# Kernel optimization log

Hardware: AMD Instinct MI355X
Metric: run time of the kernel (lower is better)

The kernel has to match this reference:

```python
import jax, jax.numpy as jnp
import numpy as np

N = 50000       # number of nodes in the batch
K = 32          # max neighbors (padded)
D = 64          # embed_dim
V = 100000      # number of users (u2e vocab)


def setup_inputs() -> dict:
    key = jax.random.key(0)
    ks = jax.random.split(key, 10)
    nodes = jax.random.randint(ks[0], (N,), 0, V)
    neigh_idx = jax.random.randint(ks[1], (N, K), 0, V)
    counts = jax.random.randint(ks[2], (N,), 1, K + 1)          # ragged lengths, >=1
    neigh_mask = jnp.arange(K)[None, :] < counts[:, None]        # [N,K] bool
    u2e = jax.random.normal(ks[3], (V, D), dtype=jnp.float32) * 0.02
    s1 = 1.0 / np.sqrt(2 * D)
    s2 = 1.0 / np.sqrt(D)
    W1 = jax.random.normal(ks[4], (2 * D, D), dtype=jnp.float32) * s1
    b1 = jnp.zeros((D,), dtype=jnp.float32)
    W2 = jax.random.normal(ks[5], (D, D), dtype=jnp.float32) * s2
    b2 = jnp.zeros((D,), dtype=jnp.float32)
    W3 = jax.random.normal(ks[6], (D, 1), dtype=jnp.float32) * s2
    b3 = jnp.zeros((1,), dtype=jnp.float32)
    return {"u2e": u2e, "W1": W1, "b1": b1, "W2": W2, "b2": b2,
            "W3": W3, "b3": b3, "nodes": nodes, "neigh_idx": neigh_idx,
            "neigh_mask": neigh_mask}


def reference(u2e, W1, b1, W2, b2, W3, b3, nodes, neigh_idx, neigh_mask):
    # Gather neighbor and center-node embeddings (the per-node loop, vectorized)
    e_u = u2e[neigh_idx]                                   # [N,K,D]
    u_rep = u2e[nodes]                                     # [N,D]
    # GraphRec attention MLP on concat([neighbor, center]) -> scalar score
    x = jnp.concatenate(
        [e_u, jnp.broadcast_to(u_rep[:, None, :], e_u.shape)], axis=-1)  # [N,K,2D]
    h = jax.nn.relu(x @ W1 + b1)                           # [N,K,D]
    h = jax.nn.relu(h @ W2 + b2)                           # [N,K,D]
    scores = (h @ W3 + b3)[..., 0]                         # [N,K]
    neg = jnp.asarray(-1e9, dtype=scores.dtype)
    att = jax.nn.softmax(jnp.where(neigh_mask, scores, neg), axis=-1)  # [N,K]
    att = att * neigh_mask.astype(att.dtype)
    # att_history = (e_u^T @ att)^T, per node: weighted neighbor sum
    out = jnp.einsum('nk,nkd->nd', att, e_u)               # [N,D]
    return out
```

## Files before the change

kernel.cpp:

```cpp
#include <hip/hip_runtime.h>
#include <hip/hip_bf16.h>

typedef __bf16 bf16x8 __attribute__((ext_vector_type(8)));
typedef __bf16 bf16x4 __attribute__((ext_vector_type(4)));
typedef float  f32x4  __attribute__((ext_vector_type(4)));

__global__ void init_flag_kernel(int* flag) { *flag = 0; }

__global__ void detect_mask_kernel(const unsigned* __restrict__ mw, int nwords,
                                   int* __restrict__ flag) {
    int any = 0;
    for (int i = blockIdx.x * blockDim.x + threadIdx.x; i < nwords;
         i += gridDim.x * blockDim.x)
        if (mw[i] > 1u) any = 1;
    if (__any(any)) {
        if ((threadIdx.x & 63) == 0) atomicOr(flag, 1);
    }
}

__global__ __launch_bounds__(256) void graphrec_agg_kernel(
    const float* __restrict__ u2e,
    const float* __restrict__ W1, const float* __restrict__ b1,
    const float* __restrict__ W2, const float* __restrict__ b2,
    const float* __restrict__ W3, const float* __restrict__ b3,
    const int* __restrict__ nodes, const int* __restrict__ neigh_idx,
    const void* __restrict__ mask, const int* __restrict__ flag,
    float* __restrict__ out, int N)
{
    __shared__ __align__(16) __bf16 w1f[16][64][8];
    __shared__ __align__(16) __bf16 w2f[8][64][8];
    __shared__ __align__(16) float  eu[4][32][64];
    __shared__ __align__(16) __bf16 afrag[4][2][2][64][8];
    __shared__ __align__(16) __bf16 urep[4][64];
    __shared__ float att_s[4][32];

    const int tid = threadIdx.x;
    const int w = tid >> 6;
    const int l = tid & 63;
    const int g = l >> 4;
    const int c = l & 15;

    for (int f = w; f < 16; f += 4) {
        int kt = f >> 2, nt = f & 3;
        int r0 = kt * 32 + g * 8, col = nt * 16 + c;
        bf16x8 t;
        #pragma unroll
        for (int i = 0; i < 8; ++i) t[i] = (__bf16)W1[(r0 + i) * 64 + col];
        *(bf16x8*)&w1f[f][l][0] = t;
    }
    for (int f = w; f < 8; f += 4) {
        int kt = f >> 2, nt = f & 3;
        int r0 = kt * 32 + g * 8, col = nt * 16 + c;
        bf16x8 t;
        #pragma unroll
        for (int i = 0; i < 8; ++i) t[i] = (__bf16)W2[(r0 + i) * 64 + col];
        *(bf16x8*)&w2f[f][l][0] = t;
    }
    __syncthreads();

    float b1v[4], b2v[4], w3v[4];
    #pragma unroll
    for (int nt = 0; nt < 4; ++nt) {
        b1v[nt] = b1[nt * 16 + c];
        b2v[nt] = b2[nt * 16 + c];
        w3v[nt] = W3[nt * 16 + c];
    }
    const float b3s = b3[0];
    const int layout8 = *flag;
    const unsigned char* m8p  = (const unsigned char*)mask;
    const int*           m32p = (const int*)mask;

    for (int n = blockIdx.x * 4 + w; n < N; n += gridDim.x * 4) {
        int vidx = 0;
        if (l < 32) vidx = neigh_idx[n * 32 + l];
        bool mv = false;
        if (l < 32) mv = layout8 ? (m8p[n * 32 + l] != 0)
                                 : (m32p[n * 32 + l] != 0);
        unsigned long long bal = __ballot(mv);

        int un = nodes[n];
        float ur = u2e[(size_t)un * 64 + l];
        urep[w][l] = (__bf16)ur;

        #pragma unroll
        for (int kb = 0; kb < 8; ++kb) {
            int k = kb * 4 + g;
            int idx = __shfl(vidx, k);
            f32x4 v = *(const f32x4*)(u2e + (size_t)idx * 64 + c * 4);
            *(f32x4*)&eu[w][k][c * 4] = v;
            int d0 = c * 4;
            bf16x4 bv;
            bv[0] = (__bf16)v[0]; bv[1] = (__bf16)v[1];
            bv[2] = (__bf16)v[2]; bv[3] = (__bf16)v[3];
            int lanep = (k & 15) + (((d0 & 31) >> 3) << 4);
            *(bf16x4*)&afrag[w][k >> 4][d0 >> 5][lanep][d0 & 7] = bv;
        }

        #pragma unroll
        for (int mt = 0; mt < 2; ++mt) {
            bf16x8 a0 = *(const bf16x8*)&afrag[w][mt][0][l][0];
            bf16x8 a1 = *(const bf16x8*)&afrag[w][mt][1][l][0];
            bf16x8 a2 = *(const bf16x8*)&urep[w][g * 8];
            bf16x8 a3 = *(const bf16x8*)&urep[w][32 + g * 8];
            #pragma unroll
            for (int nt = 0; nt < 4; ++nt) {
                f32x4 cc = {0.f, 0.f, 0.f, 0.f};
                cc = __builtin_amdgcn_mfma_f32_16x16x32_bf16(a0, *(const bf16x8*)&w1f[0 + nt][l][0], cc, 0, 0, 0);
                cc = __builtin_amdgcn_mfma_f32_16x16x32_bf16(a1, *(const bf16x8*)&w1f[4 + nt][l][0], cc, 0, 0, 0);
                cc = __builtin_amdgcn_mfma_f32_16x16x32_bf16(a2, *(const bf16x8*)&w1f[8 + nt][l][0], cc, 0, 0, 0);
                cc = __builtin_amdgcn_mfma_f32_16x16x32_bf16(a3, *(const bf16x8*)&w1f[12 + nt][l][0], cc, 0, 0, 0);
                #pragma unroll
                for (int r = 0; r < 4; ++r) {
                    float hv = fmaxf(cc[r] + b1v[nt], 0.f);
                    int lanep = g * 4 + r + ((((nt & 1) << 1) + (c >> 3)) << 4);
                    afrag[w][mt][nt >> 1][lanep][c & 7] = (__bf16)hv;
                }
            }
        }

        float p[2][4];
        #pragma unroll
        for (int mt = 0; mt < 2; ++mt) {
            bf16x8 a0 = *(const bf16x8*)&afrag[w][mt][0][l][0];
            bf16x8 a1 = *(const bf16x8*)&afrag[w][mt][1][l][0];
            float pr0 = 0.f, pr1 = 0.f, pr2 = 0.f, pr3 = 0.f;
            #pragma unroll
            for (int nt = 0; nt < 4; ++nt) {
                f32x4 cc = {0.f, 0.f, 0.f, 0.f};
                cc = __builtin_amdgcn_mfma_f32_16x16x32_bf16(a0, *(const bf16x8*)&w2f[0 + nt][l][0], cc, 0, 0, 0);
                cc = __builtin_amdgcn_mfma_f32_16x16x32_bf16(a1, *(const bf16x8*)&w2f[4 + nt][l][0], cc, 0, 0, 0);
                pr0 += fmaxf(cc[0] + b2v[nt], 0.f) * w3v[nt];
                pr1 += fmaxf(cc[1] + b2v[nt], 0.f) * w3v[nt];
                pr2 += fmaxf(cc[2] + b2v[nt], 0.f) * w3v[nt];
                pr3 += fmaxf(cc[3] + b2v[nt], 0.f) * w3v[nt];
            }
            p[mt][0] = pr0; p[mt][1] = pr1; p[mt][2] = pr2; p[mt][3] = pr3;
        }

        float s[8];
        #pragma unroll
        for (int m = 0; m < 8; ++m) {
            float v = p[m >> 2][m & 3];
            v += __shfl_xor(v, 1);
            v += __shfl_xor(v, 2);
            v += __shfl_xor(v, 4);
            v += __shfl_xor(v, 8);
            s[m] = v + b3s;
        }

        bool vald[8];
        float m8 = -1e30f;
        #pragma unroll
        for (int m = 0; m < 8; ++m) {
            int k = (m >> 2) * 16 + g * 4 + (m & 3);
            vald[m] = ((bal >> k) & 1ull) != 0;
            if (vald[m]) m8 = fmaxf(m8, s[m]);
        }
        m8 = fmaxf(m8, __shfl_xor(m8, 16));
        m8 = fmaxf(m8, __shfl_xor(m8, 32));
        float es[8], ls = 0.f;
        #pragma unroll
        for (int m = 0; m < 8; ++m) {
            es[m] = vald[m] ? __expf(s[m] - m8) : 0.f;
            ls += es[m];
        }
        ls += __shfl_xor(ls, 16);
        ls += __shfl_xor(ls, 32);
        float inv = (ls > 0.f) ? 1.f / ls : 0.f;
        if (c == 0) {
            #pragma unroll
            for (int m = 0; m < 8; ++m) {
                int k = (m >> 2) * 16 + g * 4 + (m & 3);
                att_s[w][k] = es[m] * inv;
            }
        }

        float acc = 0.f;
        #pragma unroll
        for (int k = 0; k < 32; ++k)
            acc += att_s[w][k] * eu[w][k][l];
        out[(size_t)n * 64 + l] = acc;
    }
}

extern "C" void kernel_launch(void* const* d_in, const int* in_sizes, int n_in,
                              void* d_out, int out_size, void* d_ws, size_t ws_size,
                              hipStream_t stream) {
    const float* u2e = (const float*)d_in[0];
    const float* W1  = (const float*)d_in[1];
    const float* b1  = (const float*)d_in[2];
    const float* W2  = (const float*)d_in[3];
    const float* b2  = (const float*)d_in[4];
    const float* W3  = (const float*)d_in[5];
    const float* b3  = (const float*)d_in[6];
    const int* nodes     = (const int*)d_in[7];
    const int* neigh_idx = (const int*)d_in[8];
    const void* mask     = d_in[9];

    const int N = in_sizes[7];
    int* flag = (int*)d_ws;

    init_flag_kernel<<<1, 1, 0, stream>>>(flag);
    int nwords = in_sizes[9] / 4;
    if (nwords > 100000) nwords = 100000;
    detect_mask_kernel<<<128, 256, 0, stream>>>((const unsigned*)mask, nwords, flag);

    graphrec_agg_kernel<<<1024, 256, 0, stream>>>(
        u2e, W1, b1, W2, b2, W3, b3, nodes, neigh_idx, mask, flag,
        (float*)d_out, N);
}
```

Measured before the change: 217.7 us.

## Gather neighbors from a bf16 copy of the embedding table with prefetched indices

Adds a pre-pass converting u2e to bf16 in workspace, so neighbor gathers read half the bytes. Shared memory is reorganized into padded row-major bf16 tiles, and W2 fragments move into registers. The next node's indices and mask are prefetched one iteration ahead. Grid and launch bounds change, and the flag reset becomes a memset. The final weighted sum now uses bf16 neighbor values, which lowers output precision.

```diff
diff --git a/kernel.cpp b/kernel.cpp
--- a/kernel.cpp
+++ b/kernel.cpp
@@ -4,8 +4,6 @@
 typedef __bf16 bf16x8 __attribute__((ext_vector_type(8)));
 typedef __bf16 bf16x4 __attribute__((ext_vector_type(4)));
 typedef float  f32x4  __attribute__((ext_vector_type(4)));
-
-__global__ void init_flag_kernel(int* flag) { *flag = 0; }
 
 __global__ void detect_mask_kernel(const unsigned* __restrict__ mw, int nwords,
                                    int* __restrict__ flag) {
@@ -18,8 +16,24 @@
     }
 }
 
-__global__ __launch_bounds__(256) void graphrec_agg_kernel(
-    const float* __restrict__ u2e,
+__global__ void cvt_bf16_kernel(const float* __restrict__ src,
+                                __bf16* __restrict__ dst, int n) {
+    for (int i = (blockIdx.x * blockDim.x + threadIdx.x) * 8; i < n;
+         i += gridDim.x * blockDim.x * 8) {
+        f32x4 a = *(const f32x4*)(src + i);
+        f32x4 b = *(const f32x4*)(src + i + 4);
+        bf16x8 o;
+        o[0] = (__bf16)a[0]; o[1] = (__bf16)a[1];
+        o[2] = (__bf16)a[2]; o[3] = (__bf16)a[3];
+        o[4] = (__bf16)b[0]; o[5] = (__bf16)b[1];
+        o[6] = (__bf16)b[2]; o[7] = (__bf16)b[3];
+        *(bf16x8*)(dst + i) = o;
+    }
+}
+
+template <int BF16SRC>
+__global__ __launch_bounds__(256, 3) void graphrec_agg_kernel(
+    const float* __restrict__ u2e, const __bf16* __restrict__ tbl,
     const float* __restrict__ W1, const float* __restrict__ b1,
     const float* __restrict__ W2, const float* __restrict__ b2,
     const float* __restrict__ W3, const float* __restrict__ b3,
@@ -28,9 +42,8 @@
     float* __restrict__ out, int N)
 {
     __shared__ __align__(16) __bf16 w1f[16][64][8];
-    __shared__ __align__(16) __bf16 w2f[8][64][8];
-    __shared__ __align__(16) float  eu[4][32][64];
-    __shared__ __align__(16) __bf16 afrag[4][2][2][64][8];
+    __shared__ __align__(16) __bf16 eu16[4][32][72];
+    __shared__ __align__(16) __bf16 h1s[4][32][72];
     __shared__ __align__(16) __bf16 urep[4][64];
     __shared__ float att_s[4][32];
 
@@ -48,15 +61,16 @@
         for (int i = 0; i < 8; ++i) t[i] = (__bf16)W1[(r0 + i) * 64 + col];
         *(bf16x8*)&w1f[f][l][0] = t;
     }
-    for (int f = w; f < 8; f += 4) {
+    __syncthreads();
+
+    bf16x8 w2r[8];
+    #pragma unroll
+    for (int f = 0; f < 8; ++f) {
         int kt = f >> 2, nt = f & 3;
         int r0 = kt * 32 + g * 8, col = nt * 16 + c;
-        bf16x8 t;
-        #pragma unroll
-        for (int i = 0; i < 8; ++i) t[i] = (__bf16)W2[(r0 + i) * 64 + col];
-        *(bf16x8*)&w2f[f][l][0] = t;
-    }
-    __syncthreads();
+        #pragma unroll
+        for (int i = 0; i < 8; ++i) w2r[f][i] = (__bf16)W2[(r0 + i) * 64 + col];
+    }
 
     float b1v[4], b2v[4], w3v[4];
     #pragma unroll
@@ -70,38 +84,67 @@
     const unsigned char* m8p  = (const unsigned char*)mask;
     const int*           m32p = (const int*)mask;
 
-    for (int n = blockIdx.x * 4 + w; n < N; n += gridDim.x * 4) {
-        int vidx = 0;
-        if (l < 32) vidx = neigh_idx[n * 32 + l];
-        bool mv = false;
-        if (l < 32) mv = layout8 ? (m8p[n * 32 + l] != 0)
-                                 : (m32p[n * 32 + l] != 0);
+    const int stride = gridDim.x * 4;
+    int n = blockIdx.x * 4 + w;
+
+    int vidx = 0, un = 0;
+    bool mv = false;
+    if (n < N) {
+        if (l < 32) {
+            vidx = neigh_idx[n * 32 + l];
+            mv = layout8 ? (m8p[n * 32 + l] != 0) : (m32p[n * 32 + l] != 0);
+        }
+        un = nodes[n];
+    }
+
+    for (; n < N; n += stride) {
+        int n2 = n + stride;
+        int vidx2 = 0, un2 = 0;
+        bool mv2 = false;
+        if (n2 < N) {
+            if (l < 32) {
+                vidx2 = neigh_idx[n2 * 32 + l];
+                mv2 = layout8 ? (m8p[n2 * 32 + l] != 0) : (m32p[n2 * 32 + l] != 0);
+            }
+            un2 = nodes[n2];
+        }
+
         unsigned long long bal = __ballot(mv);
 
-        int un = nodes[n];
-        float ur = u2e[(size_t)un * 64 + l];
-        urep[w][l] = (__bf16)ur;
-
-        #pragma unroll
-        for (int kb = 0; kb < 8; ++kb) {
-            int k = kb * 4 + g;
-            int idx = __shfl(vidx, k);
-            f32x4 v = *(const f32x4*)(u2e + (size_t)idx * 64 + c * 4);
-            *(f32x4*)&eu[w][k][c * 4] = v;
-            int d0 = c * 4;
-            bf16x4 bv;
-            bv[0] = (__bf16)v[0]; bv[1] = (__bf16)v[1];
-            bv[2] = (__bf16)v[2]; bv[3] = (__bf16)v[3];
-            int lanep = (k & 15) + (((d0 & 31) >> 3) << 4);
-            *(bf16x4*)&afrag[w][k >> 4][d0 >> 5][lanep][d0 & 7] = bv;
-        }
-
+        if (BF16SRC) {
+            urep[w][l] = tbl[(size_t)un * 64 + l];
+        } else {
+            urep[w][l] = (__bf16)u2e[(size_t)un * 64 + l];
+        }
+
+        if (BF16SRC) {
+            #pragma unroll
+            for (int it = 0; it < 4; ++it) {
+                int k = it * 8 + (l >> 3);
+                int idx = __shfl(vidx, k);
+                bf16x8 v = *(const bf16x8*)(tbl + (size_t)idx * 64 + (l & 7) * 8);
+                *(bf16x8*)&eu16[w][k][(l & 7) * 8] = v;
+            }
+        } else {
+            #pragma unroll
+            for (int it = 0; it < 8; ++it) {
+                int k = it * 4 + g;
+                int idx = __shfl(vidx, k);
+                f32x4 v = *(const f32x4*)(u2e + (size_t)idx * 64 + c * 4);
+                bf16x4 bv;
+                bv[0] = (__bf16)v[0]; bv[1] = (__bf16)v[1];
+                bv[2] = (__bf16)v[2]; bv[3] = (__bf16)v[3];
+                *(bf16x4*)&eu16[w][k][c * 4] = bv;
+            }
+        }
+
+        bf16x8 a2 = *(const bf16x8*)&urep[w][g * 8];
+        bf16x8 a3 = *(const bf16x8*)&urep[w][32 + g * 8];
         #pragma unroll
         for (int mt = 0; mt < 2; ++mt) {
-            bf16x8 a0 = *(const bf16x8*)&afrag[w][mt][0][l][0];
-            bf16x8 a1 = *(const bf16x8*)&afrag[w][mt][1][l][0];
-            bf16x8 a2 = *(const bf16x8*)&urep[w][g * 8];
-            bf16x8 a3 = *(const bf16x8*)&urep[w][32 + g * 8];
+            const __bf16* arow = &eu16[w][mt * 16 + c][0];
+            bf16x8 a0 = *(const bf16x8*)(arow + g * 8);
+            bf16x8 a1 = *(const bf16x8*)(arow + 32 + g * 8);
             #pragma unroll
             for (int nt = 0; nt < 4; ++nt) {
                 f32x4 cc = {0.f, 0.f, 0.f, 0.f};
@@ -112,8 +155,7 @@
                 #pragma unroll
                 for (int r = 0; r < 4; ++r) {
                     float hv = fmaxf(cc[r] + b1v[nt], 0.f);
-                    int lanep = g * 4 + r + ((((nt & 1) << 1) + (c >> 3)) << 4);
-                    afrag[w][mt][nt >> 1][lanep][c & 7] = (__bf16)hv;
+                    h1s[w][mt * 16 + g * 4 + r][nt * 16 + c] = (__bf16)hv;
                 }
             }
         }
@@ -121,14 +163,15 @@
         float p[2][4];
         #pragma unroll
         for (int mt = 0; mt < 2; ++mt) {
-            bf16x8 a0 = *(const bf16x8*)&afrag[w][mt][0][l][0];
-            bf16x8 a1 = *(const bf16x8*)&afrag[w][mt][1][l][0];
+            const __bf16* arow = &h1s[w][mt * 16 + c][0];
+            bf16x8 a0 = *(const bf16x8*)(arow + g * 8);
+            bf16x8 a1 = *(const bf16x8*)(arow + 32 + g * 8);
             float pr0 = 0.f, pr1 = 0.f, pr2 = 0.f, pr3 = 0.f;
             #pragma unroll
             for (int nt = 0; nt < 4; ++nt) {
                 f32x4 cc = {0.f, 0.f, 0.f, 0.f};
-                cc = __builtin_amdgcn_mfma_f32_16x16x32_bf16(a0, *(const bf16x8*)&w2f[0 + nt][l][0], cc, 0, 0, 0);
-                cc = __builtin_amdgcn_mfma_f32_16x16x32_bf16(a1, *(const bf16x8*)&w2f[4 + nt][l][0], cc, 0, 0, 0);
+                cc = __builtin_amdgcn_mfma_f32_16x16x32_bf16(a0, w2r[0 + nt], cc, 0, 0, 0);
+                cc = __builtin_amdgcn_mfma_f32_16x16x32_bf16(a1, w2r[4 + nt], cc, 0, 0, 0);
                 pr0 += fmaxf(cc[0] + b2v[nt], 0.f) * w3v[nt];
                 pr1 += fmaxf(cc[1] + b2v[nt], 0.f) * w3v[nt];
                 pr2 += fmaxf(cc[2] + b2v[nt], 0.f) * w3v[nt];
@@ -178,8 +221,10 @@
         float acc = 0.f;
         #pragma unroll
         for (int k = 0; k < 32; ++k)
-            acc += att_s[w][k] * eu[w][k][l];
+            acc += att_s[w][k] * (float)eu16[w][k][l];
         out[(size_t)n * 64 + l] = acc;
+
+        vidx = vidx2; mv = mv2; un = un2;
     }
 }
 
@@ -197,15 +242,26 @@
     const int* neigh_idx = (const int*)d_in[8];
     const void* mask     = d_in[9];
 
-    const int N = in_sizes[7];
+    const int N  = in_sizes[7];
+    const int VD = in_sizes[0];
+
     int* flag = (int*)d_ws;
-
-    init_flag_kernel<<<1, 1, 0, stream>>>(flag);
+    __bf16* tbl = (__bf16*)((char*)d_ws + 256);
+    const size_t needed = 256 + (size_t)VD * sizeof(__bf16);
+    const bool use16 = (ws_size >= needed);
+
+    hipMemsetAsync(flag, 0, sizeof(int), stream);
     int nwords = in_sizes[9] / 4;
-    if (nwords > 100000) nwords = 100000;
     detect_mask_kernel<<<128, 256, 0, stream>>>((const unsigned*)mask, nwords, flag);
 
-    graphrec_agg_kernel<<<1024, 256, 0, stream>>>(
-        u2e, W1, b1, W2, b2, W3, b3, nodes, neigh_idx, mask, flag,
-        (float*)d_out, N);
-}
+    if (use16) {
+        cvt_bf16_kernel<<<2048, 256, 0, stream>>>(u2e, tbl, VD);
+        graphrec_agg_kernel<1><<<768, 256, 0, stream>>>(
+            u2e, tbl, W1, b1, W2, b2, W3, b3, nodes, neigh_idx, mask, flag,
+            (float*)d_out, N);
+    } else {
+        graphrec_agg_kernel<0><<<768, 256, 0, stream>>>(
+            u2e, (const __bf16*)u2e, W1, b1, W2, b2, W3, b3, nodes, neigh_idx,
+            mask, flag, (float*)d_out, N);
+    }
+}
```

Result: slower. 319.9 us (+47.0%).

## Software-pipeline neighbor gathers and keep W2 and embeddings in registers

Applied to the files above, without the earlier changes.

Restructures the per-node loop into a software pipeline. The next node's neighbor embeddings and center embedding are loaded into registers while the current node's MLP runs, and index and mask loads are prefetched two nodes ahead. W2 fragments and the fp32 neighbor rows move from shared memory into registers, and the bf16 shared tile becomes a single padded row-major buffer, which shrinks LDS use. The final weighted sum is computed from registers with cross-lane shuffles. Launch bounds, grid size and the flag init (now a memset) also change, and the mask-detect scan loses its cap. The trade-offs are higher register pressure, which could limit occupancy, and a full scan of the mask.

```diff
diff --git a/kernel.cpp b/kernel.cpp
--- a/kernel.cpp
+++ b/kernel.cpp
@@ -4,8 +4,6 @@
 typedef __bf16 bf16x8 __attribute__((ext_vector_type(8)));
 typedef __bf16 bf16x4 __attribute__((ext_vector_type(4)));
 typedef float  f32x4  __attribute__((ext_vector_type(4)));
-
-__global__ void init_flag_kernel(int* flag) { *flag = 0; }
 
 __global__ void detect_mask_kernel(const unsigned* __restrict__ mw, int nwords,
                                    int* __restrict__ flag) {
@@ -18,7 +16,7 @@
     }
 }
 
-__global__ __launch_bounds__(256) void graphrec_agg_kernel(
+__global__ __launch_bounds__(256, 3) void graphrec_agg_kernel(
     const float* __restrict__ u2e,
     const float* __restrict__ W1, const float* __restrict__ b1,
     const float* __restrict__ W2, const float* __restrict__ b2,
@@ -28,9 +26,7 @@
     float* __restrict__ out, int N)
 {
     __shared__ __align__(16) __bf16 w1f[16][64][8];
-    __shared__ __align__(16) __bf16 w2f[8][64][8];
-    __shared__ __align__(16) float  eu[4][32][64];
-    __shared__ __align__(16) __bf16 afrag[4][2][2][64][8];
+    __shared__ __align__(16) __bf16 tile[4][32][72];
     __shared__ __align__(16) __bf16 urep[4][64];
     __shared__ float att_s[4][32];
 
@@ -48,15 +44,16 @@
         for (int i = 0; i < 8; ++i) t[i] = (__bf16)W1[(r0 + i) * 64 + col];
         *(bf16x8*)&w1f[f][l][0] = t;
     }
-    for (int f = w; f < 8; f += 4) {
+    __syncthreads();
+
+    bf16x8 w2r[8];
+    #pragma unroll
+    for (int f = 0; f < 8; ++f) {
         int kt = f >> 2, nt = f & 3;
         int r0 = kt * 32 + g * 8, col = nt * 16 + c;
-        bf16x8 t;
-        #pragma unroll
-        for (int i = 0; i < 8; ++i) t[i] = (__bf16)W2[(r0 + i) * 64 + col];
-        *(bf16x8*)&w2f[f][l][0] = t;
-    }
-    __syncthreads();
+        #pragma unroll
+        for (int i = 0; i < 8; ++i) w2r[f][i] = (__bf16)W2[(r0 + i) * 64 + col];
+    }
 
     float b1v[4], b2v[4], w3v[4];
     #pragma unroll
@@ -70,38 +67,77 @@
     const unsigned char* m8p  = (const unsigned char*)mask;
     const int*           m32p = (const int*)mask;
 
-    for (int n = blockIdx.x * 4 + w; n < N; n += gridDim.x * 4) {
-        int vidx = 0;
-        if (l < 32) vidx = neigh_idx[n * 32 + l];
-        bool mv = false;
-        if (l < 32) mv = layout8 ? (m8p[n * 32 + l] != 0)
-                                 : (m32p[n * 32 + l] != 0);
-        unsigned long long bal = __ballot(mv);
-
-        int un = nodes[n];
-        float ur = u2e[(size_t)un * 64 + l];
-        urep[w][l] = (__bf16)ur;
-
+    const int stride = gridDim.x * 4;
+    int nA = blockIdx.x * 4 + w;
+    int nB = nA + stride;
+
+    int vidxA = 0, unA = 0; bool mvA = false;
+    if (nA < N) {
+        if (l < 32) {
+            int o = nA * 32 + l;
+            vidxA = neigh_idx[o];
+            mvA = layout8 ? (m8p[o] != 0) : (m32p[o] != 0);
+        }
+        unA = nodes[nA];
+    }
+    int vidxB = 0, unB = 0; bool mvB = false;
+    if (nB < N) {
+        if (l < 32) {
+            int o = nB * 32 + l;
+            vidxB = neigh_idx[o];
+            mvB = layout8 ? (m8p[o] != 0) : (m32p[o] != 0);
+        }
+        unB = nodes[nB];
+    }
+
+    f32x4 rr[8]; float urv = 0.f;
+    if (nA < N) {
+        #pragma unroll
+        for (int kb = 0; kb < 8; ++kb) {
+            int idx = __shfl(vidxA, kb * 4 + g);
+            rr[kb] = *(const f32x4*)(u2e + (size_t)idx * 64 + c * 4);
+        }
+        urv = u2e[(size_t)unA * 64 + l];
+    }
+
+    for (; nA < N; nA += stride, nB += stride) {
+        int nC = nB + stride;
+        int vidxC = 0, unC = 0; bool mvC = false;
+        if (nC < N) {
+            if (l < 32) {
+                int o = nC * 32 + l;
+                vidxC = neigh_idx[o];
+                mvC = layout8 ? (m8p[o] != 0) : (m32p[o] != 0);
+            }
+            unC = nodes[nC];
+        }
+
+        unsigned long long bal = __ballot(mvA);
+        urep[w][l] = (__bf16)urv;
         #pragma unroll
         for (int kb = 0; kb < 8; ++kb) {
             int k = kb * 4 + g;
-            int idx = __shfl(vidx, k);
-            f32x4 v = *(const f32x4*)(u2e + (size_t)idx * 64 + c * 4);
-            *(f32x4*)&eu[w][k][c * 4] = v;
-            int d0 = c * 4;
             bf16x4 bv;
-            bv[0] = (__bf16)v[0]; bv[1] = (__bf16)v[1];
-            bv[2] = (__bf16)v[2]; bv[3] = (__bf16)v[3];
-            int lanep = (k & 15) + (((d0 & 31) >> 3) << 4);
-            *(bf16x4*)&afrag[w][k >> 4][d0 >> 5][lanep][d0 & 7] = bv;
-        }
-
+            bv[0] = (__bf16)rr[kb][0]; bv[1] = (__bf16)rr[kb][1];
+            bv[2] = (__bf16)rr[kb][2]; bv[3] = (__bf16)rr[kb][3];
+            *(bf16x4*)&tile[w][k][c * 4] = bv;
+        }
+
+        f32x4 rn[8]; float urvn;
+        #pragma unroll
+        for (int kb = 0; kb < 8; ++kb) {
+            int idx = __shfl(vidxB, kb * 4 + g);
+            rn[kb] = *(const f32x4*)(u2e + (size_t)idx * 64 + c * 4);
+        }
+        urvn = u2e[(size_t)unB * 64 + l];
+
+        bf16x8 a2 = *(const bf16x8*)&urep[w][g * 8];
+        bf16x8 a3 = *(const bf16x8*)&urep[w][32 + g * 8];
         #pragma unroll
         for (int mt = 0; mt < 2; ++mt) {
-            bf16x8 a0 = *(const bf16x8*)&afrag[w][mt][0][l][0];
-            bf16x8 a1 = *(const bf16x8*)&afrag[w][mt][1][l][0];
-            bf16x8 a2 = *(const bf16x8*)&urep[w][g * 8];
-            bf16x8 a3 = *(const bf16x8*)&urep[w][32 + g * 8];
+            const __bf16* arow = &tile[w][mt * 16 + c][0];
+            bf16x8 a0 = *(const bf16x8*)(arow + g * 8);
+            bf16x8 a1 = *(const bf16x8*)(arow + 32 + g * 8);
             #pragma unroll
             for (int nt = 0; nt < 4; ++nt) {
                 f32x4 cc = {0.f, 0.f, 0.f, 0.f};
@@ -112,8 +148,7 @@
                 #pragma unroll
                 for (int r = 0; r < 4; ++r) {
                     float hv = fmaxf(cc[r] + b1v[nt], 0.f);
-                    int lanep = g * 4 + r + ((((nt & 1) << 1) + (c >> 3)) << 4);
-                    afrag[w][mt][nt >> 1][lanep][c & 7] = (__bf16)hv;
+                    tile[w][mt * 16 + g * 4 + r][nt * 16 + c] = (__bf16)hv;
                 }
             }
         }
@@ -121,14 +156,15 @@
         float p[2][4];
         #pragma unroll
         for (int mt = 0; mt < 2; ++mt) {
-            bf16x8 a0 = *(const bf16x8*)&afrag[w][mt][0][l][0];
-            bf16x8 a1 = *(const bf16x8*)&afrag[w][mt][1][l][0];
+            const __bf16* arow = &tile[w][mt * 16 + c][0];
+            bf16x8 a0 = *(const bf16x8*)(arow + g * 8);
+            bf16x8 a1 = *(const bf16x8*)(arow + 32 + g * 8);
             float pr0 = 0.f, pr1 = 0.f, pr2 = 0.f, pr3 = 0.f;
             #pragma unroll
             for (int nt = 0; nt < 4; ++nt) {
                 f32x4 cc = {0.f, 0.f, 0.f, 0.f};
-                cc = __builtin_amdgcn_mfma_f32_16x16x32_bf16(a0, *(const bf16x8*)&w2f[0 + nt][l][0], cc, 0, 0, 0);
-                cc = __builtin_amdgcn_mfma_f32_16x16x32_bf16(a1, *(const bf16x8*)&w2f[4 + nt][l][0], cc, 0, 0, 0);
+                cc = __builtin_amdgcn_mfma_f32_16x16x32_bf16(a0, w2r[0 + nt], cc, 0, 0, 0);
+                cc = __builtin_amdgcn_mfma_f32_16x16x32_bf16(a1, w2r[4 + nt], cc, 0, 0, 0);
                 pr0 += fmaxf(cc[0] + b2v[nt], 0.f) * w3v[nt];
                 pr1 += fmaxf(cc[1] + b2v[nt], 0.f) * w3v[nt];
                 pr2 += fmaxf(cc[2] + b2v[nt], 0.f) * w3v[nt];
@@ -175,11 +211,27 @@
             }
         }
 
-        float acc = 0.f;
-        #pragma unroll
-        for (int k = 0; k < 32; ++k)
-            acc += att_s[w][k] * eu[w][k][l];
-        out[(size_t)n * 64 + l] = acc;
+        float o0 = 0.f, o1 = 0.f, o2 = 0.f, o3 = 0.f;
+        #pragma unroll
+        for (int kb = 0; kb < 8; ++kb) {
+            float a = att_s[w][kb * 4 + g];
+            o0 += a * rr[kb][0]; o1 += a * rr[kb][1];
+            o2 += a * rr[kb][2]; o3 += a * rr[kb][3];
+        }
+        o0 += __shfl_xor(o0, 16); o0 += __shfl_xor(o0, 32);
+        o1 += __shfl_xor(o1, 16); o1 += __shfl_xor(o1, 32);
+        o2 += __shfl_xor(o2, 16); o2 += __shfl_xor(o2, 32);
+        o3 += __shfl_xor(o3, 16); o3 += __shfl_xor(o3, 32);
+        if (g == 0) {
+            f32x4 ov = {o0, o1, o2, o3};
+            *(f32x4*)(out + (size_t)nA * 64 + c * 4) = ov;
+        }
+
+        #pragma unroll
+        for (int kb = 0; kb < 8; ++kb) rr[kb] = rn[kb];
+        urv = urvn;
+        mvA = mvB;
+        vidxB = vidxC; mvB = mvC; unB = unC;
     }
 }
 
@@ -200,12 +252,11 @@
     const int N = in_sizes[7];
     int* flag = (int*)d_ws;
 
-    init_flag_kernel<<<1, 1, 0, stream>>>(flag);
+    hipMemsetAsync(flag, 0, sizeof(int), stream);
     int nwords = in_sizes[9] / 4;
-    if (nwords > 100000) nwords = 100000;
     detect_mask_kernel<<<128, 256, 0, stream>>>((const unsigned*)mask, nwords, flag);
 
-    graphrec_agg_kernel<<<1024, 256, 0, stream>>>(
+    graphrec_agg_kernel<<<768, 256, 0, stream>>>(
         u2e, W1, b1, W2, b2, W3, b3, nodes, neigh_idx, mask, flag,
         (float*)d_out, N);
 }
```

New measurement: 234.1 us. +7.5%, slower.
